# Kernel optimization log

Hardware: AMD Instinct MI355X
Metric: run time of the kernel (lower is better)

The kernel has to match this reference:

```python
import jax, jax.numpy as jnp
import numpy as np

E, M, B, S = 1024, 256, 4, 2048
LN_EPS = 1e-5

def _l2norm(x):
    # F.normalize(p=2, dim=-1, eps=1e-12)
    n = jnp.linalg.norm(x, axis=-1, keepdims=True)
    return x / jnp.maximum(n, 1e-12)

def _layernorm(x, g, b):
    mu = jnp.mean(x, axis=-1, keepdims=True)
    var = jnp.var(x, axis=-1, keepdims=True)
    return (x - mu) * jax.lax.rsqrt(var + LN_EPS) * g + b

def setup_inputs() -> dict:
    key = jax.random.key(0)
    ks = jax.random.split(key, 16)
    s = 0.02
    inp = {
        'x': jax.random.normal(ks[0], (B, S, E), jnp.float32),
        'memory': jnp.zeros((B, M, M), jnp.float32),
        'w_k': jax.random.normal(ks[1], (M, E), jnp.float32) * s,
        'b_k': jnp.zeros((M,), jnp.float32),
        'w_q': jax.random.normal(ks[2], (M, E), jnp.float32) * s,
        'b_q': jnp.zeros((M,), jnp.float32),
        'w_v': jax.random.normal(ks[3], (M, E), jnp.float32) * s,
        'b_v': jnp.zeros((M,), jnp.float32),
        'w_out': jax.random.normal(ks[4], (E, M), jnp.float32) * s,
        'b_out': jnp.zeros((E,), jnp.float32),
        'w_gw': jax.random.normal(ks[5], (1, E), jnp.float32) * s,
        'b_gw': jnp.full((1,), -2.0, jnp.float32),
        'w_gf': jax.random.normal(ks[6], (1, E), jnp.float32) * s,
        'b_gf': jnp.full((1,), 2.0, jnp.float32),
        'ln1_g': jnp.ones((E,), jnp.float32),
        'ln1_b': jnp.zeros((E,), jnp.float32),
        'ln2_g': jnp.ones((E,), jnp.float32),
        'ln2_b': jnp.zeros((E,), jnp.float32),
        'w_f1': jax.random.normal(ks[7], (4 * E, E), jnp.float32) * s,
        'b_f1': jnp.zeros((4 * E,), jnp.float32),
        'w_f2': jax.random.normal(ks[8], (E, 4 * E), jnp.float32) * s,
        'b_f2': jnp.zeros((E,), jnp.float32),
    }
    return inp

def reference(x, memory, w_k, b_k, w_q, b_q, w_v, b_v, w_out, b_out,
              w_gw, b_gw, w_gf, b_gf, ln1_g, ln1_b, ln2_g, ln2_b,
              w_f1, b_f1, w_f2, b_f2):
    xn = _layernorm(x, ln1_g, ln1_b)                      # [B,S,E]
    k_all = _l2norm(xn @ w_k.T + b_k)                     # [B,S,M]
    q_all = _l2norm(xn @ w_q.T + b_q)                     # [B,S,M]
    v_all = jnp.tanh(xn @ w_v.T + b_v)                    # [B,S,M]
    beta_all = jax.nn.sigmoid(xn @ w_gw.T + b_gw)         # [B,S,1]
    decay_all = jax.nn.sigmoid(xn @ w_gf.T + b_gf)        # [B,S,1]

    def step(mem, inps):
        k, q, v, beta, decay = inps                       # k,q,v:[B,M]; beta,decay:[B,1]
        readout = jnp.einsum('bij,bj->bi', mem, q)        # read BEFORE update
        assoc = v[:, :, None] * k[:, None, :]             # [B,M,M] outer product
        mem = decay[:, :, None] * mem + beta[:, :, None] * assoc
        return mem, readout

    seq = (jnp.swapaxes(k_all, 0, 1), jnp.swapaxes(q_all, 0, 1),
           jnp.swapaxes(v_all, 0, 1), jnp.swapaxes(beta_all, 0, 1),
           jnp.swapaxes(decay_all, 0, 1))
    new_memory, readouts = jax.lax.scan(step, memory, seq)  # readouts: [S,B,M]
    stacked = jnp.swapaxes(readouts, 0, 1)                  # [B,S,M]
    mixer_out = stacked @ w_out.T + b_out                   # [B,S,E]

    x = x + mixer_out
    h = _layernorm(x, ln2_g, ln2_b)
    ffn = jax.nn.gelu(h @ w_f1.T + b_f1, approximate=False) @ w_f2.T + b_f2
    x = x + ffn
    return (x, new_memory)
```

## Files before the change

kernel.cpp:

```cpp
#include <hip/hip_runtime.h>
#include <stdint.h>

#define E_DIM 1024
#define M_DIM 256
#define B_DIM 4
#define S_DIM 2048
#define NTOK  8192
#define CHUNK 64
#define NCHUNK 32
#define NCB   128

typedef unsigned short u16;
typedef unsigned int   u32;
typedef __attribute__((ext_vector_type(8))) short short8;
typedef __attribute__((ext_vector_type(4))) float floatx4;

#define OFF_WKQV   ((size_t)0)
#define OFF_WOUT   ((size_t)1572864)
#define OFF_WF1    ((size_t)2097152)
#define OFF_WF2    ((size_t)10485760)
#define OFF_BKQV   ((size_t)18874368)
#define OFF_BETA   ((size_t)18877440)
#define OFF_DECAY  ((size_t)18910208)
#define OFF_P      ((size_t)18942976)
#define OFF_WW     ((size_t)18976256)
#define OFF_ABUF   ((size_t)19009024)
#define OFF_XN     ((size_t)21106176)
#define OFF_KQV    ((size_t)37883392)
#define OFF_T      ((size_t)63049216)
#define OFF_STATES ((size_t)96603648)
#define OFF_RO     ((size_t)130158080)
#define OFF_H      OFF_XN
#define OFF_Y1     OFF_T
#define OFF_G      OFF_STATES
#define OFF_P2     OFF_XN

__device__ __forceinline__ u16 f2bf(float f) {
    union { float f; u32 u; } a; a.f = f;
    u32 u = a.u;
    return (u16)((u + 0x7fffu + ((u >> 16) & 1u)) >> 16);
}
__device__ __forceinline__ u32 pack2bf(float a, float b) {
    return (u32)f2bf(a) | ((u32)f2bf(b) << 16);
}
__device__ __forceinline__ float sigmoidf_(float x) { return 1.0f / (1.0f + expf(-x)); }

__device__ __forceinline__ void gload_lds16(const u16* g, u16* l) {
    __builtin_amdgcn_global_load_lds((const __attribute__((address_space(1))) void*)g,
                                     (__attribute__((address_space(3))) void*)l, 16, 0, 0);
}

__device__ __forceinline__ int sw_slot(int idx) {
    return ((idx & 3) ^ ((idx >> 3) & 3)) * 8;
}
__device__ __forceinline__ int sw_read(int row, int kc) {
    return row * 32 + ((kc ^ ((row >> 1) & 3)) << 3);
}

__device__ __forceinline__ void block_reduce_2(float& a, float& b, float* red, int t) {
#pragma unroll
    for (int o = 32; o > 0; o >>= 1) { a += __shfl_xor(a, o); b += __shfl_xor(b, o); }
    if ((t & 63) == 0) { red[t >> 6] = a; red[4 + (t >> 6)] = b; }
    __syncthreads();
    a = red[0] + red[1] + red[2] + red[3];
    b = red[4] + red[5] + red[6] + red[7];
    __syncthreads();
}

__device__ __forceinline__ uint2 cvt4(float4 v) {
    uint2 o; o.x = pack2bf(v.x, v.y); o.y = pack2bf(v.z, v.w); return o;
}
__global__ void convert_weights(const float4* __restrict__ wk, const float4* __restrict__ wq,
                                const float4* __restrict__ wv, const float4* __restrict__ wo,
                                const float4* __restrict__ wf1in, const float4* __restrict__ wf2in,
                                const float* __restrict__ bk, const float* __restrict__ bq,
                                const float* __restrict__ bv,
                                uint2* __restrict__ wkqv, uint2* __restrict__ wout,
                                uint2* __restrict__ wf1, uint2* __restrict__ wf2,
                                float* __restrict__ bkqv) {
    int b = blockIdx.x, t = threadIdx.x;
    if (b < 768) {
        int i = b * 256 + t;
        int sec = i >> 16, off = i & 65535;
        const float4* s = (sec == 0) ? wk : ((sec == 1) ? wq : wv);
        wkqv[i] = cvt4(s[off]);
    } else if (b < 1024) {
        int i = (b - 768) * 256 + t;
        wout[i] = cvt4(wo[i]);
    } else if (b < 5120) {
        int i = (b - 1024) * 256 + t;
        wf1[i] = cvt4(wf1in[i]);
    } else if (b < 9216) {
        int i = (b - 5120) * 256 + t;
        wf2[i] = cvt4(wf2in[i]);
    } else {
        bkqv[t] = bk[t]; bkqv[256 + t] = bq[t]; bkqv[512 + t] = bv[t];
    }
}

__global__ __launch_bounds__(256) void ln1_gates(
    const float* __restrict__ x, const float* __restrict__ g, const float* __restrict__ b,
    const float* __restrict__ wgw, const float* __restrict__ bgw,
    const float* __restrict__ wgf, const float* __restrict__ bgf,
    u16* __restrict__ xn, float* __restrict__ beta, float* __restrict__ decay)
{
    __shared__ float red[8];
    const int row = blockIdx.x;
    const int t = threadIdx.x;
    const float4 v = ((const float4*)(x + (size_t)row * E_DIM))[t];
    float s  = v.x + v.y + v.z + v.w;
    float ss = v.x * v.x + v.y * v.y + v.z * v.z + v.w * v.w;
    block_reduce_2(s, ss, red, t);
    const float mean = s * (1.0f / E_DIM);
    const float var  = ss * (1.0f / E_DIM) - mean * mean;
    const float rstd = rsqrtf(var + 1e-5f);
    const float4 gg = ((const float4*)g)[t];
    const float4 bb = ((const float4*)b)[t];
    float4 xnv;
    xnv.x = (v.x - mean) * rstd * gg.x + bb.x;
    xnv.y = (v.y - mean) * rstd * gg.y + bb.y;
    xnv.z = (v.z - mean) * rstd * gg.z + bb.z;
    xnv.w = (v.w - mean) * rstd * gg.w + bb.w;
    uint2 o; o.x = pack2bf(xnv.x, xnv.y); o.y = pack2bf(xnv.z, xnv.w);
    ((uint2*)(xn + (size_t)row * E_DIM))[t] = o;
    const float4 w1 = ((const float4*)wgw)[t];
    const float4 w2 = ((const float4*)wgf)[t];
    float dg = xnv.x * w1.x + xnv.y * w1.y + xnv.z * w1.z + xnv.w * w1.w;
    float df = xnv.x * w2.x + xnv.y * w2.y + xnv.z * w2.z + xnv.w * w2.w;
    block_reduce_2(dg, df, red, t);
    if (t == 0) {
        beta[row]  = sigmoidf_(dg + bgw[0]);
        decay[row] = sigmoidf_(df + bgf[0]);
    }
}

__global__ __launch_bounds__(256) void ln2_kernel(
    const float* __restrict__ y1, const float* __restrict__ g, const float* __restrict__ b,
    u16* __restrict__ h)
{
    __shared__ float red[8];
    const int row = blockIdx.x;
    const int t = threadIdx.x;
    const float4 v = ((const float4*)(y1 + (size_t)row * E_DIM))[t];
    float s  = v.x + v.y + v.z + v.w;
    float ss = v.x * v.x + v.y * v.y + v.z * v.z + v.w * v.w;
    block_reduce_2(s, ss, red, t);
    const float mean = s * (1.0f / E_DIM);
    const float var  = ss * (1.0f / E_DIM) - mean * mean;
    const float rstd = rsqrtf(var + 1e-5f);
    const float4 gg = ((const float4*)g)[t];
    const float4 bb = ((const float4*)b)[t];
    float4 xnv;
    xnv.x = (v.x - mean) * rstd * gg.x + bb.x;
    xnv.y = (v.y - mean) * rstd * gg.y + bb.y;
    xnv.z = (v.z - mean) * rstd * gg.z + bb.z;
    xnv.w = (v.w - mean) * rstd * gg.w + bb.w;
    uint2 o; o.x = pack2bf(xnv.x, xnv.y); o.y = pack2bf(xnv.z, xnv.w);
    ((uint2*)(h + (size_t)row * E_DIM))[t] = o;
}

__global__ __launch_bounds__(256) void kqv_act(float* __restrict__ pA,
                                               const float* __restrict__ pB,
                                               const float* __restrict__ bias) {
    __shared__ float red[8];
    const int row = blockIdx.x;
    const int t = threadIdx.x;
    float* p = pA + (size_t)row * 768;
    const float* q = pB + (size_t)row * 768;
    float kv = p[t]       + q[t]       + bias[t];
    float qv = p[256 + t] + q[256 + t] + bias[256 + t];
    float vv = p[512 + t] + q[512 + t] + bias[512 + t];
    float sk = kv * kv, sq = qv * qv;
    block_reduce_2(sk, sq, red, t);
    float nk = fmaxf(sqrtf(sk), 1e-12f);
    float nq = fmaxf(sqrtf(sq), 1e-12f);
    p[t]       = kv / nk;
    p[256 + t] = qv / nq;
    p[512 + t] = tanhf(vv);
}

__global__ void chunk_prep(const float* __restrict__ beta, const float* __restrict__ decay,
                           float* __restrict__ P, float* __restrict__ ww) {
    int cb = blockIdx.x;
    int b = cb >> 5, c = cb & 31;
    int tb = b * S_DIM + c * CHUNK;
    int j = threadIdx.x;
    __shared__ float d[64], bt[64], Ps[65];
    d[j]  = decay[tb + j];
    bt[j] = beta[tb + j];
    __syncthreads();
    if (j == 0) {
        float p = 1.0f; Ps[0] = 1.0f;
        for (int i = 0; i < 64; i++) { p *= d[i]; Ps[i + 1] = p; }
    }
    __syncthreads();
    P[cb * 65 + j] = Ps[j];
    if (j == 0) P[cb * 65 + 64] = Ps[64];
    ww[cb * 64 + j] = bt[j] / Ps[j + 1];
}

__global__ __launch_bounds__(256) void t_kernel(const float* __restrict__ kqv,
                                                const float* __restrict__ P,
                                                const float* __restrict__ ww,
                                                float* __restrict__ T) {
    int cb = blockIdx.y;
    int tile = blockIdx.x;
    int r0 = (tile >> 2) * 64, c0 = (tile & 3) * 64;
    int b = cb >> 5, c = cb & 31;
    int tb = b * S_DIM + c * CHUNK;
    float p64 = P[cb * 65 + 64];
    __shared__ float Vs[64][65], Ks[64][65];
    int t = threadIdx.x;
#pragma unroll
    for (int i = 0; i < 16; i++) {
        int idx = t + i * 256; int j = idx >> 6, col = idx & 63;
        float sc = ww[cb * 64 + j] * p64;
        Vs[j][col] = kqv[(size_t)(tb + j) * 768 + 512 + r0 + col] * sc;
        Ks[j][col] = kqv[(size_t)(tb + j) * 768 + 0   + c0 + col];
    }
    __syncthreads();
    int tr = t >> 4, tc = t & 15;
    float a[4][4] = {};
    for (int j = 0; j < 64; j++) {
        float vv[4], kk[4];
#pragma unroll
        for (int r = 0; r < 4; r++)  vv[r] = Vs[j][tr * 4 + r];
#pragma unroll
        for (int cc = 0; cc < 4; cc++) kk[cc] = Ks[j][tc * 4 + cc];
#pragma unroll
        for (int r = 0; r < 4; r++)
#pragma unroll
            for (int cc = 0; cc < 4; cc++) a[r][cc] += vv[r] * kk[cc];
    }
#pragma unroll
    for (int r = 0; r < 4; r++)
#pragma unroll
        for (int cc = 0; cc < 4; cc++)
            T[(size_t)cb * 65536 + (size_t)(r0 + tr * 4 + r) * 256 + (c0 + tc * 4 + cc)] = a[r][cc];
}

__global__ void mem_scan(const float* __restrict__ mem0, const float* __restrict__ T,
                         const float* __restrict__ P, float* __restrict__ states,
                         float* __restrict__ memOut) {
    int gid = blockIdx.x * 256 + threadIdx.x;
    int b = gid >> 16; int e = gid & 65535;
    float s = mem0[gid];
    for (int c = 0; c < NCHUNK; c++) {
        int cb = b * NCHUNK + c;
        states[(size_t)cb * 65536 + e] = s;
        s = P[cb * 65 + 64] * s + T[(size_t)cb * 65536 + e];
    }
    memOut[gid] = s;
}

__global__ __launch_bounds__(256) void qk_attn(const float* __restrict__ kqv,
                                               const float* __restrict__ P,
                                               const float* __restrict__ ww,
                                               float* __restrict__ Abuf) {
    int cb = blockIdx.x;
    int b = cb >> 5, c = cb & 31;
    int tb = b * S_DIM + c * CHUNK;
    __shared__ float Qs[64][65], Ks[64][65];
    int t = threadIdx.x;
    int tr = t >> 4, tc = t & 15;
    float acc[4][4] = {};
    for (int kt = 0; kt < 4; kt++) {
        __syncthreads();
#pragma unroll
        for (int i = 0; i < 16; i++) {
            int idx = t + i * 256; int rr = idx >> 6, cc2 = idx & 63;
            Qs[rr][cc2] = kqv[(size_t)(tb + rr) * 768 + 256 + kt * 64 + cc2];
            Ks[rr][cc2] = kqv[(size_t)(tb + rr) * 768 + 0   + kt * 64 + cc2];
        }
        __syncthreads();
        for (int kk = 0; kk < 64; kk++) {
            float qq[4], kx[4];
#pragma unroll
            for (int r = 0; r < 4; r++)  qq[r] = Qs[tr * 4 + r][kk];
#pragma unroll
            for (int cc = 0; cc < 4; cc++) kx[cc] = Ks[tc * 4 + cc][kk];
#pragma unroll
            for (int r = 0; r < 4; r++)
#pragma unroll
                for (int cc = 0; cc < 4; cc++) acc[r][cc] += qq[r] * kx[cc];
        }
    }
#pragma unroll
    for (int r = 0; r < 4; r++) {
#pragma unroll
        for (int cc = 0; cc < 4; cc++) {
            int i = tr * 4 + r, j = tc * 4 + cc;
            float v = (j < i) ? acc[r][cc] * (P[cb * 65 + i] * ww[cb * 64 + j]) : 0.0f;
            Abuf[(size_t)cb * 4096 + i * 64 + j] = v;
        }
    }
}

__global__ __launch_bounds__(256) void readout_k(const float* __restrict__ kqv,
                                                 const float* __restrict__ Abuf,
                                                 const float* __restrict__ states,
                                                 const float* __restrict__ P,
                                                 u16* __restrict__ ro) {
    int cb = blockIdx.y;
    int rt = blockIdx.x;
    int b = cb >> 5, c = cb & 31;
    int tb = b * S_DIM + c * CHUNK;
    int r0 = rt * 64;
    __shared__ float As[64][65], Vs[64][65], Qs[64][65], Ms[64][65];
    int t = threadIdx.x;
    int tr = t >> 4, tc = t & 15;
#pragma unroll
    for (int i = 0; i < 16; i++) {
        int idx = t + i * 256; int rr = idx >> 6, cc2 = idx & 63;
        As[rr][cc2] = Abuf[(size_t)cb * 4096 + rr * 64 + cc2];
        Vs[rr][cc2] = kqv[(size_t)(tb + rr) * 768 + 512 + r0 + cc2];
    }
    __syncthreads();
    float acc[4][4] = {};
    for (int j = 0; j < 64; j++) {
        float aa[4], vv[4];
#pragma unroll
        for (int r = 0; r < 4; r++)  aa[r] = As[tr * 4 + r][j];
#pragma unroll
        for (int cc = 0; cc < 4; cc++) vv[cc] = Vs[j][tc * 4 + cc];
#pragma unroll
        for (int r = 0; r < 4; r++)
#pragma unroll
            for (int cc = 0; cc < 4; cc++) acc[r][cc] += aa[r] * vv[cc];
    }
    float acc2[4][4] = {};
    for (int kt = 0; kt < 4; kt++) {
        __syncthreads();
#pragma unroll
        for (int i = 0; i < 16; i++) {
            int idx = t + i * 256; int rr = idx >> 6, cc2 = idx & 63;
            Qs[rr][cc2] = kqv[(size_t)(tb + rr) * 768 + 256 + kt * 64 + cc2];
            Ms[rr][cc2] = states[(size_t)cb * 65536 + (size_t)(r0 + rr) * 256 + kt * 64 + cc2];
        }
        __syncthreads();
        for (int kk = 0; kk < 64; kk++) {
            float qq[4], mm[4];
#pragma unroll
            for (int r = 0; r < 4; r++)  qq[r] = Qs[tr * 4 + r][kk];
#pragma unroll
            for (int cc = 0; cc < 4; cc++) mm[cc] = Ms[tc * 4 + cc][kk];
#pragma unroll
            for (int r = 0; r < 4; r++)
#pragma unroll
                for (int cc = 0; cc < 4; cc++) acc2[r][cc] += qq[r] * mm[cc];
        }
    }
#pragma unroll
    for (int r = 0; r < 4; r++) {
#pragma unroll
        for (int cc = 0; cc < 4; cc++) {
            int i = tr * 4 + r;
            float val = acc[r][cc] + P[cb * 65 + i] * acc2[r][cc];
            ro[(size_t)(tb + i) * 256 + r0 + tc * 4 + cc] = f2bf(val);
        }
    }
}

__global__ __launch_bounds__(256) void combine_k(float4* __restrict__ out,
                                                 const float4* __restrict__ part) {
    int i = blockIdx.x * 256 + threadIdx.x;
    float4 a = out[i], b = part[i];
    a.x += b.x; a.y += b.y; a.z += b.z; a.w += b.w;
    out[i] = a;
}

#define EPI_BIAS   0
#define EPI_RESID  1
#define EPI_GELU   2
#define EPI_SPART  3
#define EPI_SRESID 4

template<int EPI, int BM, int MY, int SQH, int SQW>
__global__ __launch_bounds__(256) void gemm_bt(
    const u16* __restrict__ A, int lda,
    const u16* __restrict__ B, int ldb,
    const float* __restrict__ bias,
    const float* __restrict__ resid,
    float* __restrict__ outF, u16* __restrict__ outB,
    int ldc, int K, float* __restrict__ part)
{
    constexpr int MI = BM / 32;
    __shared__ u16 As[2][BM * 32];
    __shared__ u16 Bs[2][128 * 32];
    const int t = threadIdx.x;
    const int lane = t & 63;
    const int w = t >> 6;
    const int waveM = (w >> 1) * (BM / 2);
    const int waveN = (w & 1) * 64;

    int bx, by;
    if (MY == 0) {
        bx = blockIdx.x; by = blockIdx.y;
    } else {
        const u32 NX = gridDim.x;
        u32 flat = blockIdx.x + NX * blockIdx.y;
        u32 xcd = flat & 7;
        u32 local = flat >> 3;
        u32 perBand = (u32)SQH * NX;
        u32 band = local / perBand;
        u32 rem  = local - band * perBand;
        u32 sq   = rem / (SQH * SQW);
        u32 wloc = rem - sq * (SQH * SQW);
        u32 wy = wloc / SQW, wx = wloc - wy * SQW;
        by = xcd * MY + band * SQH + wy;
        bx = sq * SQW + wx;
    }

    const int m0 = by * BM;
    const int n0 = bx * 128;
    const size_t koff = (size_t)blockIdx.z * K;

    const int sr = t >> 2, scw = sw_slot(t);
    const u16* Ag0 = A + (size_t)(m0 + sr) * lda + koff + scw;
    const u16* Ag1 = A + (size_t)(m0 + 64 + sr) * lda + koff + scw;
    const u16* Bg0 = B + (size_t)(n0 + sr) * ldb + koff + scw;
    const u16* Bg1 = B + (size_t)(n0 + 64 + sr) * ldb + koff + scw;

    floatx4 acc[MI][4] = {};

    const int kc = lane >> 4;
    const int rsel = lane & 15;
    const int NK = K >> 5;

    gload_lds16(Ag0, As[0] + t * 8);
    if (BM == 128) gload_lds16(Ag1, As[0] + (t + 256) * 8);
    gload_lds16(Bg0, Bs[0] + t * 8);
    gload_lds16(Bg1, Bs[0] + (t + 256) * 8);

    for (int kt = 0; kt < NK; kt++) {
        __syncthreads();
        const int cur = kt & 1;
        if (kt + 1 < NK) {
            const int kof = (kt + 1) * 32;
            gload_lds16(Ag0 + kof, As[cur ^ 1] + t * 8);
            if (BM == 128) gload_lds16(Ag1 + kof, As[cur ^ 1] + (t + 256) * 8);
            gload_lds16(Bg0 + kof, Bs[cur ^ 1] + t * 8);
            gload_lds16(Bg1 + kof, Bs[cur ^ 1] + (t + 256) * 8);
        }
        short8 af[MI], bfr[4];
#pragma unroll
        for (int i = 0; i < MI; i++)
            af[i] = *(const short8*)(As[cur] + sw_read(waveM + i * 16 + rsel, kc));
#pragma unroll
        for (int j = 0; j < 4; j++)
            bfr[j] = *(const short8*)(Bs[cur] + sw_read(waveN + j * 16 + rsel, kc));
#pragma unroll
        for (int i = 0; i < MI; i++)
#pragma unroll
            for (int j = 0; j < 4; j++)
                acc[i][j] = __builtin_amdgcn_mfma_f32_16x16x32_bf16(af[i], bfr[j], acc[i][j], 0, 0, 0);
    }

    const bool zmain = (blockIdx.z == 0);
    const int rbase = (lane >> 4) * 4;
#pragma unroll
    for (int i = 0; i < MI; i++) {
#pragma unroll
        for (int j = 0; j < 4; j++) {
            const int col = n0 + waveN + j * 16 + rsel;
            float bv = 0.0f;
            if (EPI == EPI_BIAS || EPI == EPI_RESID || EPI == EPI_GELU) bv = bias[col];
            if (EPI == EPI_SRESID && zmain) bv = bias[col];
#pragma unroll
            for (int r = 0; r < 4; r++) {
                const int row = m0 + waveM + i * 16 + rbase + r;
                const size_t oidx = (size_t)row * ldc + col;
                float v = acc[i][j][r] + bv;
                if (EPI == EPI_BIAS) {
                    outF[oidx] = v;
                } else if (EPI == EPI_RESID) {
                    outF[oidx] = v + resid[oidx];
                } else if (EPI == EPI_GELU) {
                    float gl = 0.5f * v * (1.0f + erff(v * 0.70710678118654752f));
                    outB[oidx] = f2bf(gl);
                } else if (EPI == EPI_SPART) {
                    (zmain ? outF : part)[oidx] = v;
                } else {
                    if (zmain) outF[oidx] = v + resid[oidx];
                    else       part[oidx] = v;
                }
            }
        }
    }
}

__device__ __forceinline__ void g8_frags(const u16* LA, const u16* LB,
                                         int wm, int wn, int rsel, int kc,
                                         short8 (&af)[8], short8 (&bv)[4]) {
#pragma unroll
    for (int i = 0; i < 8; i++)
        af[i] = *(const short8*)(LA + sw_read(wm * 128 + i * 16 + rsel, kc));
#pragma unroll
    for (int j = 0; j < 4; j++)
        bv[j] = *(const short8*)(LB + sw_read(wn * 64 + j * 16 + rsel, kc));
}
__device__ __forceinline__ void g8_mfma(short8 (&af)[8], short8 (&bv)[4], floatx4 (&acc)[8][4]) {
    __builtin_amdgcn_s_setprio(1);
#pragma unroll
    for (int i = 0; i < 8; i++)
#pragma unroll
        for (int j = 0; j < 4; j++)
            acc[i][j] = __builtin_amdgcn_mfma_f32_16x16x32_bf16(af[i], bv[j], acc[i][j], 0, 0, 0);
    __builtin_amdgcn_s_setprio(0);
}

template<int EPI, int MY, int SQH, int SQW>
__global__ __launch_bounds__(512, 2) void gemm8(
    const u16* __restrict__ A, int lda,
    const u16* __restrict__ B, int ldb,
    const float* __restrict__ bias,
    const float* __restrict__ resid,
    float* __restrict__ outF, u16* __restrict__ outB,
    int ldc, int K, float* __restrict__ part)
{
    __shared__ u16 L[4][2][8192];
    const int t = threadIdx.x;
    const int lane = t & 63;
    const int w = t >> 6;
    const int wm = w >> 2;
    const int wn = w & 3;
    const int kc = lane >> 4;
    const int rsel = lane & 15;

    int bx, by;
    {
        const u32 NX = gridDim.x;
        u32 flat = blockIdx.x + NX * blockIdx.y;
        u32 xcd = flat & 7;
        u32 local = flat >> 3;
        u32 perBand = (u32)SQH * NX;
        u32 band = local / perBand;
        u32 rem  = local - band * perBand;
        u32 sq   = rem / (SQH * SQW);
        u32 wloc = rem - sq * (SQH * SQW);
        u32 wy = wloc / SQW, wx = wloc - wy * SQW;
        by = xcd * MY + band * SQH + wy;
        bx = sq * SQW + wx;
    }
    const int m0 = by * 256;
    const int n0 = bx * 256;
    const size_t koff = (size_t)blockIdx.z * K;

    const int srow = t >> 2;
    const int scw  = sw_slot(t);
    const u16* Asrc = A + (size_t)(m0 + srow) * lda + koff + scw;
    const u16* Bsrc = B + (size_t)(n0 + srow) * ldb + koff + scw;

    floatx4 acc[8][4] = {};
    const int NR = (K >> 5);

    auto STAGE = [&](int r) {
        const int ko = r * 32;
        u16* la = &L[r & 3][0][0];
        u16* lb = &L[r & 3][1][0];
        gload_lds16(Asrc + ko, la + t * 8);
        gload_lds16(Asrc + (size_t)128 * lda + ko, la + 4096 + t * 8);
        gload_lds16(Bsrc + ko, lb + t * 8);
        gload_lds16(Bsrc + (size_t)128 * ldb + ko, lb + 4096 + t * 8);
    };

    STAGE(0); STAGE(1); STAGE(2);
    asm volatile("s_waitcnt vmcnt(8)" ::: "memory");
    __builtin_amdgcn_s_barrier();
    __builtin_amdgcn_sched_barrier(0);

    for (int p = 0; p < NR; ++p) {
        short8 af[8], bv[4];
        g8_frags(&L[p & 3][0][0], &L[p & 3][1][0], wm, wn, rsel, kc, af, bv);
        if (p + 1 < NR) {
            if (p + 2 < NR) { asm volatile("s_waitcnt vmcnt(4)" ::: "memory"); }
            else            { asm volatile("s_waitcnt vmcnt(0)" ::: "memory"); }
        }
        __builtin_amdgcn_s_barrier();
        __builtin_amdgcn_sched_barrier(0);
        if (p + 3 < NR) STAGE(p + 3);
        asm volatile("s_waitcnt lgkmcnt(0)" ::: "memory");
        __builtin_amdgcn_sched_barrier(0);
        g8_mfma(af, bv, acc);
    }

    const bool zmain = (blockIdx.z == 0);
    const int rbase = kc * 4;
#pragma unroll
    for (int i = 0; i < 8; i++) {
#pragma unroll
        for (int j = 0; j < 4; j++) {
            const int col = n0 + wn * 64 + j * 16 + rsel;
            float bvv = 0.0f;
            if (EPI == EPI_BIAS || EPI == EPI_RESID || EPI == EPI_GELU) bvv = bias[col];
            if (EPI == EPI_SRESID && zmain) bvv = bias[col];
#pragma unroll
            for (int r = 0; r < 4; r++) {
                const int row = m0 + wm * 128 + i * 16 + rbase + r;
                const size_t oidx = (size_t)row * ldc + col;
                float v = acc[i][j][r] + bvv;
                if (EPI == EPI_BIAS) {
                    outF[oidx] = v;
                } else if (EPI == EPI_RESID) {
                    outF[oidx] = v + resid[oidx];
                } else if (EPI == EPI_GELU) {
                    float gl = 0.5f * v * (1.0f + erff(v * 0.70710678118654752f));
                    outB[oidx] = f2bf(gl);
                } else if (EPI == EPI_SPART) {
                    (zmain ? outF : part)[oidx] = v;
                } else {
                    if (zmain) outF[oidx] = v + resid[oidx];
                    else       part[oidx] = v;
                }
            }
        }
    }
}

extern "C" void kernel_launch(void* const* d_in, const int* in_sizes, int n_in,
                              void* d_out, int out_size, void* d_ws, size_t ws_size,
                              hipStream_t stream) {
    const float* x     = (const float*)d_in[0];
    const float* mem0  = (const float*)d_in[1];
    const float* w_k   = (const float*)d_in[2];
    const float* b_k   = (const float*)d_in[3];
    const float* w_q   = (const float*)d_in[4];
    const float* b_q   = (const float*)d_in[5];
    const float* w_v   = (const float*)d_in[6];
    const float* b_v   = (const float*)d_in[7];
    const float* w_out = (const float*)d_in[8];
    const float* b_out = (const float*)d_in[9];
    const float* w_gw  = (const float*)d_in[10];
    const float* b_gw  = (const float*)d_in[11];
    const float* w_gf  = (const float*)d_in[12];
    const float* b_gf  = (const float*)d_in[13];
    const float* ln1g  = (const float*)d_in[14];
    const float* ln1b  = (const float*)d_in[15];
    const float* ln2g  = (const float*)d_in[16];
    const float* ln2b  = (const float*)d_in[17];
    const float* w_f1  = (const float*)d_in[18];
    const float* b_f1  = (const float*)d_in[19];
    const float* w_f2  = (const float*)d_in[20];
    const float* b_f2  = (const float*)d_in[21];

    char* ws = (char*)d_ws;
    u16*   wkqv  = (u16*)(ws + OFF_WKQV);
    u16*   wout  = (u16*)(ws + OFF_WOUT);
    u16*   wf1   = (u16*)(ws + OFF_WF1);
    u16*   wf2   = (u16*)(ws + OFF_WF2);
    float* bkqv  = (float*)(ws + OFF_BKQV);
    float* beta  = (float*)(ws + OFF_BETA);
    float* decay = (float*)(ws + OFF_DECAY);
    float* P     = (float*)(ws + OFF_P);
    float* ww    = (float*)(ws + OFF_WW);
    float* Abuf  = (float*)(ws + OFF_ABUF);
    u16*   xn    = (u16*)(ws + OFF_XN);
    float* kqv   = (float*)(ws + OFF_KQV);
    float* kqvPB = (float*)(ws + OFF_T);
    float* T     = (float*)(ws + OFF_T);
    float* states= (float*)(ws + OFF_STATES);
    u16*   ro    = (u16*)(ws + OFF_RO);
    u16*   h     = (u16*)(ws + OFF_H);
    float* y1    = (float*)(ws + OFF_Y1);
    u16*   g     = (u16*)(ws + OFF_G);
    float* p2    = (float*)(ws + OFF_P2);

    float* out_x   = (float*)d_out;
    float* out_mem = out_x + (size_t)NTOK * E_DIM;

    convert_weights<<<9217, 256, 0, stream>>>(
        (const float4*)w_k, (const float4*)w_q, (const float4*)w_v,
        (const float4*)w_out, (const float4*)w_f1, (const float4*)w_f2,
        b_k, b_q, b_v,
        (uint2*)wkqv, (uint2*)wout, (uint2*)wf1, (uint2*)wf2, bkqv);

    ln1_gates<<<NTOK, 256, 0, stream>>>(x, ln1g, ln1b, w_gw, b_gw, w_gf, b_gf, xn, beta, decay);

    gemm_bt<EPI_SPART, 128, 0, 0, 0><<<dim3(6, 64, 2), 256, 0, stream>>>(
        xn, 1024, wkqv, 1024, nullptr, nullptr, kqv, nullptr, 768, 512, kqvPB);
    kqv_act<<<NTOK, 256, 0, stream>>>(kqv, kqvPB, bkqv);

    chunk_prep<<<NCB, 64, 0, stream>>>(beta, decay, P, ww);
    t_kernel<<<dim3(16, NCB), 256, 0, stream>>>(kqv, P, ww, T);
    mem_scan<<<1024, 256, 0, stream>>>(mem0, T, P, states, out_mem);
    qk_attn<<<NCB, 256, 0, stream>>>(kqv, P, ww, Abuf);
    readout_k<<<dim3(4, NCB), 256, 0, stream>>>(kqv, Abuf, states, P, ro);

    gemm_bt<EPI_RESID, 64, 0, 0, 0><<<dim3(8, 128), 256, 0, stream>>>(
        ro, 256, wout, 256, b_out, x, y1, nullptr, 1024, 256, nullptr);

    ln2_kernel<<<NTOK, 256, 0, stream>>>(y1, ln2g, ln2b, h);
    gemm8<EPI_GELU, 4, 4, 4><<<dim3(16, 32), 512, 0, stream>>>(
        h, 1024, wf1, 1024, b_f1, nullptr, nullptr, g, 4096, 1024, nullptr);
    gemm8<EPI_SRESID, 4, 4, 4><<<dim3(4, 32, 2), 512, 0, stream>>>(
        g, 4096, wf2, 4096, b_f2, y1, out_x, nullptr, 1024, 2048, p2);
    combine_k<<<8192, 256, 0, stream>>>((float4*)out_x, (const float4*)p2);
}
```

Measured before the change: 520.9 us.

## Shrink FFN GEMM tiles to 256x128 with 3-stage LDS ring and fast GELU

The FFN GEMM kernel now uses 256x128 tiles with 8 waves in a 4x2 grid. Each wave owns a 64x64 sub-tile, so the accumulator array is half its previous size. The pipeline drops from four LDS stages to three, and launch bounds are raised to allow four blocks per CU, aiming at better occupancy and latency hiding. The price is less operand reuse per tile and more tiles to schedule. Separately, the erff-based GELU epilogue is replaced by an Abramowitz-Stegun polynomial approximation using a hardware reciprocal and fast exp, which trades a small amount of accuracy for cheaper epilogue math.

```diff
diff --git a/kernel.cpp b/kernel.cpp
--- a/kernel.cpp
+++ b/kernel.cpp
@@ -44,6 +44,17 @@
     return (u32)f2bf(a) | ((u32)f2bf(b) << 16);
 }
 __device__ __forceinline__ float sigmoidf_(float x) { return 1.0f / (1.0f + expf(-x)); }
+
+__device__ __forceinline__ float gelu_fast(float v) {
+    float z = __builtin_fabsf(v) * 0.70710678118654752f;
+    float t = __builtin_amdgcn_rcpf(1.0f + 0.3275911f * z);
+    float p = t * (0.254829592f + t * (-0.284496736f +
+              t * (1.421413741f + t * (-1.453152027f + t * 1.061405429f))));
+    float e = __expf(-z * z);
+    float erfz = 1.0f - p * e;
+    float s = (v < 0.0f) ? -erfz : erfz;
+    return 0.5f * v * (1.0f + s);
+}
 
 __device__ __forceinline__ void gload_lds16(const u16* g, u16* l) {
     __builtin_amdgcn_global_load_lds((const __attribute__((address_space(1))) void*)g,
@@ -476,8 +487,7 @@
                 } else if (EPI == EPI_RESID) {
                     outF[oidx] = v + resid[oidx];
                 } else if (EPI == EPI_GELU) {
-                    float gl = 0.5f * v * (1.0f + erff(v * 0.70710678118654752f));
-                    outB[oidx] = f2bf(gl);
+                    outB[oidx] = f2bf(gelu_fast(v));
                 } else if (EPI == EPI_SPART) {
                     (zmain ? outF : part)[oidx] = v;
                 } else {
@@ -489,28 +499,8 @@
     }
 }
 
-__device__ __forceinline__ void g8_frags(const u16* LA, const u16* LB,
-                                         int wm, int wn, int rsel, int kc,
-                                         short8 (&af)[8], short8 (&bv)[4]) {
-#pragma unroll
-    for (int i = 0; i < 8; i++)
-        af[i] = *(const short8*)(LA + sw_read(wm * 128 + i * 16 + rsel, kc));
-#pragma unroll
-    for (int j = 0; j < 4; j++)
-        bv[j] = *(const short8*)(LB + sw_read(wn * 64 + j * 16 + rsel, kc));
-}
-__device__ __forceinline__ void g8_mfma(short8 (&af)[8], short8 (&bv)[4], floatx4 (&acc)[8][4]) {
-    __builtin_amdgcn_s_setprio(1);
-#pragma unroll
-    for (int i = 0; i < 8; i++)
-#pragma unroll
-        for (int j = 0; j < 4; j++)
-            acc[i][j] = __builtin_amdgcn_mfma_f32_16x16x32_bf16(af[i], bv[j], acc[i][j], 0, 0, 0);
-    __builtin_amdgcn_s_setprio(0);
-}
-
 template<int EPI, int MY, int SQH, int SQW>
-__global__ __launch_bounds__(512, 2) void gemm8(
+__global__ __launch_bounds__(512, 4) void gemm_hk(
     const u16* __restrict__ A, int lda,
     const u16* __restrict__ B, int ldb,
     const float* __restrict__ bias,
@@ -518,12 +508,12 @@
     float* __restrict__ outF, u16* __restrict__ outB,
     int ldc, int K, float* __restrict__ part)
 {
-    __shared__ u16 L[4][2][8192];
+    __shared__ u16 L[3][12288];
     const int t = threadIdx.x;
     const int lane = t & 63;
     const int w = t >> 6;
-    const int wm = w >> 2;
-    const int wn = w & 3;
+    const int waveM = (w >> 1) * 64;
+    const int waveN = (w & 1) * 64;
     const int kc = lane >> 4;
     const int rsel = lane & 15;
 
@@ -543,7 +533,7 @@
         bx = sq * SQW + wx;
     }
     const int m0 = by * 256;
-    const int n0 = bx * 256;
+    const int n0 = bx * 128;
     const size_t koff = (size_t)blockIdx.z * K;
 
     const int srow = t >> 2;
@@ -551,52 +541,67 @@
     const u16* Asrc = A + (size_t)(m0 + srow) * lda + koff + scw;
     const u16* Bsrc = B + (size_t)(n0 + srow) * ldb + koff + scw;
 
-    floatx4 acc[8][4] = {};
-    const int NR = (K >> 5);
-
-    auto STAGE = [&](int r) {
+    floatx4 acc[4][4] = {};
+    const int NR = K >> 5;
+
+    auto STAGE = [&](int r, int slot) {
         const int ko = r * 32;
-        u16* la = &L[r & 3][0][0];
-        u16* lb = &L[r & 3][1][0];
+        u16* la = &L[slot][0];
+        u16* lb = &L[slot][8192];
         gload_lds16(Asrc + ko, la + t * 8);
         gload_lds16(Asrc + (size_t)128 * lda + ko, la + 4096 + t * 8);
         gload_lds16(Bsrc + ko, lb + t * 8);
-        gload_lds16(Bsrc + (size_t)128 * ldb + ko, lb + 4096 + t * 8);
     };
 
-    STAGE(0); STAGE(1); STAGE(2);
-    asm volatile("s_waitcnt vmcnt(8)" ::: "memory");
+    STAGE(0, 0); STAGE(1, 1);
+    asm volatile("s_waitcnt vmcnt(3)" ::: "memory");
     __builtin_amdgcn_s_barrier();
     __builtin_amdgcn_sched_barrier(0);
 
+    int sc = 0;
     for (int p = 0; p < NR; ++p) {
-        short8 af[8], bv[4];
-        g8_frags(&L[p & 3][0][0], &L[p & 3][1][0], wm, wn, rsel, kc, af, bv);
+        short8 af[4], bv[4];
+#pragma unroll
+        for (int i = 0; i < 4; i++)
+            af[i] = *(const short8*)(&L[sc][0] + sw_read(waveM + i * 16 + rsel, kc));
+#pragma unroll
+        for (int j = 0; j < 4; j++)
+            bv[j] = *(const short8*)(&L[sc][8192] + sw_read(waveN + j * 16 + rsel, kc));
+        if (p + 2 < NR) {
+            int ss = sc + 2; if (ss >= 3) ss -= 3;
+            STAGE(p + 2, ss);
+        }
         if (p + 1 < NR) {
-            if (p + 2 < NR) { asm volatile("s_waitcnt vmcnt(4)" ::: "memory"); }
+            if (p + 2 < NR) { asm volatile("s_waitcnt vmcnt(3)" ::: "memory"); }
             else            { asm volatile("s_waitcnt vmcnt(0)" ::: "memory"); }
-        }
-        __builtin_amdgcn_s_barrier();
-        __builtin_amdgcn_sched_barrier(0);
-        if (p + 3 < NR) STAGE(p + 3);
+            __builtin_amdgcn_s_barrier();
+            __builtin_amdgcn_sched_barrier(0);
+        }
         asm volatile("s_waitcnt lgkmcnt(0)" ::: "memory");
         __builtin_amdgcn_sched_barrier(0);
-        g8_mfma(af, bv, acc);
+        __builtin_amdgcn_s_setprio(1);
+#pragma unroll
+        for (int i = 0; i < 4; i++)
+#pragma unroll
+            for (int j = 0; j < 4; j++)
+                acc[i][j] = __builtin_amdgcn_mfma_f32_16x16x32_bf16(af[i], bv[j], acc[i][j], 0, 0, 0);
+        __builtin_amdgcn_s_setprio(0);
+        sc = (sc + 1 == 3) ? 0 : sc + 1;
     }
 
     const bool zmain = (blockIdx.z == 0);
     const int rbase = kc * 4;
 #pragma unroll
-    for (int i = 0; i < 8; i++) {
+    for (int i = 0; i < 4; i++) {
 #pragma unroll
         for (int j = 0; j < 4; j++) {
-            const int col = n0 + wn * 64 + j * 16 + rsel;
+            const int col = n0 + waveN + j * 16 + rsel;
             float bvv = 0.0f;
             if (EPI == EPI_BIAS || EPI == EPI_RESID || EPI == EPI_GELU) bvv = bias[col];
             if (EPI == EPI_SRESID && zmain) bvv = bias[col];
 #pragma unroll
             for (int r = 0; r < 4; r++) {
-                const int row = m0 + wm * 128 + i * 16 + rbase + r;
+                const int row = m0 + waveM + i * 16 + rbase + r;
                 const size_t oidx = (size_t)row * ldc + col;
                 float v = acc[i][j][r] + bvv;
                 if (EPI == EPI_BIAS) {
@@ -604,8 +609,7 @@
                 } else if (EPI == EPI_RESID) {
                     outF[oidx] = v + resid[oidx];
                 } else if (EPI == EPI_GELU) {
-                    float gl = 0.5f * v * (1.0f + erff(v * 0.70710678118654752f));
-                    outB[oidx] = f2bf(gl);
+                    outB[oidx] = f2bf(gelu_fast(v));
                 } else if (EPI == EPI_SPART) {
                     (zmain ? outF : part)[oidx] = v;
                 } else {
@@ -690,9 +694,9 @@
         ro, 256, wout, 256, b_out, x, y1, nullptr, 1024, 256, nullptr);
 
     ln2_kernel<<<NTOK, 256, 0, stream>>>(y1, ln2g, ln2b, h);
-    gemm8<EPI_GELU, 4, 4, 4><<<dim3(16, 32), 512, 0, stream>>>(
+    gemm_hk<EPI_GELU, 4, 4, 8><<<dim3(32, 32), 512, 0, stream>>>(
         h, 1024, wf1, 1024, b_f1, nullptr, nullptr, g, 4096, 1024, nullptr);
-    gemm8<EPI_SRESID, 4, 4, 4><<<dim3(4, 32, 2), 512, 0, stream>>>(
+    gemm_hk<EPI_SRESID, 4, 4, 8><<<dim3(8, 32, 2), 512, 0, stream>>>(
         g, 4096, wf2, 4096, b_f2, y1, out_x, nullptr, 1024, 2048, p2);
     combine_k<<<8192, 256, 0, stream>>>((float4*)out_x, (const float4*)p2);
 }
```

After: 484.8 us. 6.9% less time.
